# Performance work log

Measured on AMD Instinct MI355X. Metric: run time of the kernel, lower is better.

The kernel has to match this reference:

```python
import jax, jax.numpy as jnp
import numpy as np

N, DEG, D_FEAT, D_OUT = 50000, 32, 128, 256

def setup_inputs() -> dict:
    key = jax.random.key(0)
    k1, k2, k3 = jax.random.split(key, 3)
    features = jax.random.normal(k1, (N, D_FEAT), dtype=jnp.float32)
    edge_look_up = jax.random.randint(k2, (N, DEG), 0, N, dtype=jnp.int64)
    # glorot-uniform kernel, shape (2*D_FEAT, D_OUT)
    limit = np.sqrt(6.0 / (2 * D_FEAT + D_OUT)).astype(np.float32)
    kernel = jax.random.uniform(k3, (2 * D_FEAT, D_OUT), dtype=jnp.float32,
                                minval=-limit, maxval=limit)
    return {"features": features, "edge_look_up": edge_look_up, "kernel": kernel}

def reference(features, edge_look_up, kernel):
    # [1] neighborhood aggregation: gather neighbor features and mean-reduce
    neigh = features[edge_look_up]          # [N, DEG, D_FEAT] (irregular gather)
    agg = jnp.mean(neigh, axis=1)           # [N, D_FEAT]
    # [2] concat self features with aggregated neighbor vectors
    out = jnp.concatenate([features, agg], axis=-1)  # [N, 2*D_FEAT]
    # [4] dense matmul + [5] relu activation
    return jax.nn.relu(out @ kernel)        # [N, D_OUT]
```

## Files before the change

kernel.cpp:

```cpp
#include <hip/hip_runtime.h>

#define NN  50000
#define DEG 32
#define DF  128
#define DO  256
#define FEAT4 (NN * DF / 4)

typedef __bf16 bf16x8 __attribute__((ext_vector_type(8)));
typedef float  f32x4  __attribute__((ext_vector_type(4)));
typedef float  f32x2  __attribute__((ext_vector_type(2)));
typedef unsigned short u16x8 __attribute__((ext_vector_type(8)));

#if defined(__has_builtin)
#if __has_builtin(__builtin_amdgcn_cvt_pk_f32_fp8) && __has_builtin(__builtin_amdgcn_cvt_pk_fp8_f32)
#define HW_FP8 1
#endif
#endif
#ifndef HW_FP8
#define HW_FP8 0
#endif

__device__ __forceinline__ unsigned short f2bf(float f) {
    unsigned u = __float_as_uint(f);
    u += 0x7FFF + ((u >> 16) & 1);
    return (unsigned short)(u >> 16);
}

#if !HW_FP8
__device__ __forceinline__ unsigned enc1_fp8(float f) {
    unsigned u = __float_as_uint(f);
    unsigned s = (u >> 31) << 7;
    float a = fabsf(f);
    if (!(a > 0.f)) return s;
    if (a >= 448.f) return s | 0x7E;
    u = __float_as_uint(a);
    int e = (int)((u >> 23) & 255) - 127;
    if (e < -6) {
        unsigned m = (unsigned)(a * 512.f + 0.5f);
        if (m >= 8) return s | 0x08;
        return s | m;
    }
    unsigned mant = (u >> 20) & 7;
    unsigned rnd  = ((u >> 19) & 1) & (((u & 0x7FFFF) != 0) | ((u >> 20) & 1));
    unsigned enc  = ((unsigned)(e + 7) << 3) | mant;
    return s | (enc + rnd);
}
__device__ __forceinline__ float dec1_fp8(unsigned b) {
    unsigned s = (b >> 7) & 1, e = (b >> 3) & 15, m = b & 7;
    float v = (e == 0) ? (float)m * 0.001953125f
                       : __uint_as_float(((e - 7 + 127) << 23) | (m << 20));
    return s ? -v : v;
}
#endif

__device__ __forceinline__ unsigned enc4_fp8(float4 v) {
#if HW_FP8
    int pk = 0;
    pk = __builtin_amdgcn_cvt_pk_fp8_f32(v.x, v.y, pk, false);
    pk = __builtin_amdgcn_cvt_pk_fp8_f32(v.z, v.w, pk, true);
    return (unsigned)pk;
#else
    return enc1_fp8(v.x) | (enc1_fp8(v.y) << 8) | (enc1_fp8(v.z) << 16) | (enc1_fp8(v.w) << 24);
#endif
}

__global__ __launch_bounds__(256) void convert_kernel(
    const float* __restrict__ feat, const float* __restrict__ W,
    unsigned* __restrict__ feat8, unsigned short* __restrict__ featb,
    unsigned short* __restrict__ Wt)
{
    const int gid = blockIdx.x * 256 + threadIdx.x;
    if (gid < FEAT4) {
        const float4 v = ((const float4*)feat)[gid];
        feat8[gid] = enc4_fp8(v);
        ushort4 o;
        o.x = f2bf(v.x); o.y = f2bf(v.y); o.z = f2bf(v.z); o.w = f2bf(v.w);
        ((ushort4*)featb)[gid] = o;
    } else {
        const int t = gid - FEAT4;
        if (t < DO * DO) {
            const int n = t >> 8, k = t & 255;
            Wt[n * DO + k] = f2bf(W[k * DO + n]);
        }
    }
}

__global__ __launch_bounds__(256) void agg_kernel(
    const unsigned* __restrict__ feat8,
    const int*      __restrict__ edges,
    unsigned short* __restrict__ aggb)
{
    const int node = blockIdx.x * 16 + (threadIdx.x >> 4);
    const int l    = threadIdx.x & 15;
    const int* e   = edges + node * DEG;

    float a[8] = {0.f, 0.f, 0.f, 0.f, 0.f, 0.f, 0.f, 0.f};
    #pragma unroll
    for (int d = 0; d < DEG; ++d) {
        const int idx = e[d];
        const uint2 pk = *(const uint2*)(feat8 + (size_t)idx * (DF / 4) + l * 2);
#if HW_FP8
        const f32x2 v0 = __builtin_amdgcn_cvt_pk_f32_fp8((int)pk.x, false);
        const f32x2 v1 = __builtin_amdgcn_cvt_pk_f32_fp8((int)pk.x, true);
        const f32x2 v2 = __builtin_amdgcn_cvt_pk_f32_fp8((int)pk.y, false);
        const f32x2 v3 = __builtin_amdgcn_cvt_pk_f32_fp8((int)pk.y, true);
        a[0] += v0[0]; a[1] += v0[1]; a[2] += v1[0]; a[3] += v1[1];
        a[4] += v2[0]; a[5] += v2[1]; a[6] += v3[0]; a[7] += v3[1];
#else
        #pragma unroll
        for (int j = 0; j < 4; ++j) a[j]     += dec1_fp8((pk.x >> (8 * j)) & 255);
        #pragma unroll
        for (int j = 0; j < 4; ++j) a[4 + j] += dec1_fp8((pk.y >> (8 * j)) & 255);
#endif
    }

    const float s = 1.0f / (float)DEG;
    u16x8 o;
    #pragma unroll
    for (int j = 0; j < 8; ++j) o[j] = f2bf(a[j] * s);
    *(u16x8*)(aggb + (size_t)node * DF + l * 8) = o;
}

#define BM  64
#define BN  256
#define LDT 72

__global__ __launch_bounds__(512) void gemm_kernel(
    const unsigned short* __restrict__ featb,
    const unsigned short* __restrict__ aggb,
    const unsigned short* __restrict__ Wt,
    float*                __restrict__ out)
{
    __shared__ __align__(16) unsigned short Asw[BM * LDT];
    __shared__ __align__(16) unsigned short Bsw[BN * LDT];

    const int tid = threadIdx.x;
    const int m0  = blockIdx.x * BM;

    const int wave = tid >> 6, lane = tid & 63;
    const int quad = lane >> 4, lr = lane & 15;
    const int wm   = (wave & 1) * 32;
    const int wn   = (wave >> 1) * 64;

    f32x4 acc[2][4] = {};

    for (int kc = 0; kc < 4; ++kc) {
        const unsigned short* srcA = (kc < 2) ? (featb + kc * 64)
                                              : (aggb + (kc - 2) * 64);

        if (kc) __syncthreads();

        {
            const int r = tid >> 3;
            const int c = (tid & 7) * 8;
            int node = m0 + r;
            if (node >= NN) node = NN - 1;
            *(u16x8*)(Asw + r * LDT + c) =
                *(const u16x8*)(srcA + (size_t)node * DF + c);
        }

        #pragma unroll
        for (int it = 0; it < 4; ++it) {
            const int sidx = it * 512 + tid;
            const int r = sidx >> 3;
            const int c = (sidx & 7) * 8;
            *(u16x8*)(Bsw + r * LDT + c) =
                *(const u16x8*)(Wt + (size_t)r * DO + kc * 64 + c);
        }

        __syncthreads();

        #pragma unroll
        for (int kk = 0; kk < 64; kk += 32) {
            const int kb = kk + quad * 8;
            bf16x8 af[2], bfr[4];
            #pragma unroll
            for (int i = 0; i < 2; ++i)
                af[i] = *(const bf16x8*)(Asw + (wm + i * 16 + lr) * LDT + kb);
            #pragma unroll
            for (int i = 0; i < 4; ++i)
                bfr[i] = *(const bf16x8*)(Bsw + (wn + i * 16 + lr) * LDT + kb);
            #pragma unroll
            for (int mi = 0; mi < 2; ++mi)
                #pragma unroll
                for (int ni = 0; ni < 4; ++ni)
                    acc[mi][ni] = __builtin_amdgcn_mfma_f32_16x16x32_bf16(
                        af[mi], bfr[ni], acc[mi][ni], 0, 0, 0);
        }
    }

    #pragma unroll
    for (int mi = 0; mi < 2; ++mi) {
        #pragma unroll
        for (int r = 0; r < 4; ++r) {
            const int row = m0 + wm + mi * 16 + quad * 4 + r;
            if (row < NN) {
                #pragma unroll
                for (int ni = 0; ni < 4; ++ni) {
                    out[(size_t)row * DO + wn + ni * 16 + lr] =
                        fmaxf(acc[mi][ni][r], 0.f);
                }
            }
        }
    }
}

extern "C" void kernel_launch(void* const* d_in, const int* in_sizes, int n_in,
                              void* d_out, int out_size, void* d_ws, size_t ws_size,
                              hipStream_t stream)
{
    const float* feat  = (const float*)d_in[0];
    const int*   edges = (const int*)d_in[1];
    const float* W     = (const float*)d_in[2];
    float*       out   = (float*)d_out;

    unsigned short* aggb  = (unsigned short*)d_ws;
    unsigned*       feat8 = (unsigned*)(aggb + (size_t)NN * DF);
    unsigned short* featb = (unsigned short*)(feat8 + (size_t)NN * DF / 4);
    unsigned short* Wt    = featb + (size_t)NN * DF;

    convert_kernel<<<(FEAT4 + DO * DO + 255) / 256, 256, 0, stream>>>(
        feat, W, feat8, featb, Wt);
    agg_kernel<<<NN / 16, 256, 0, stream>>>(feat8, edges, aggb);

    gemm_kernel<<<(NN + BM - 1) / BM, 512, 0, stream>>>(featb, aggb, Wt, out);
}
```

Measured before the change: 124.6 us.

## Convert self features to bf16 inside GEMM and stage output through LDS

```diff
diff --git a/kernel.cpp b/kernel.cpp
--- a/kernel.cpp
+++ b/kernel.cpp
@@ -66,16 +66,12 @@
 
 __global__ __launch_bounds__(256) void convert_kernel(
     const float* __restrict__ feat, const float* __restrict__ W,
-    unsigned* __restrict__ feat8, unsigned short* __restrict__ featb,
-    unsigned short* __restrict__ Wt)
+    unsigned* __restrict__ feat8, unsigned short* __restrict__ Wt)
 {
     const int gid = blockIdx.x * 256 + threadIdx.x;
     if (gid < FEAT4) {
         const float4 v = ((const float4*)feat)[gid];
         feat8[gid] = enc4_fp8(v);
-        ushort4 o;
-        o.x = f2bf(v.x); o.y = f2bf(v.y); o.z = f2bf(v.z); o.w = f2bf(v.w);
-        ((ushort4*)featb)[gid] = o;
     } else {
         const int t = gid - FEAT4;
         if (t < DO * DO) {
@@ -124,9 +120,10 @@
 #define BM  64
 #define BN  256
 #define LDT 72
+#define LDP 68
 
 __global__ __launch_bounds__(512) void gemm_kernel(
-    const unsigned short* __restrict__ featb,
+    const float*          __restrict__ feat,
     const unsigned short* __restrict__ aggb,
     const unsigned short* __restrict__ Wt,
     float*                __restrict__ out)
@@ -145,9 +142,6 @@
     f32x4 acc[2][4] = {};
 
     for (int kc = 0; kc < 4; ++kc) {
-        const unsigned short* srcA = (kc < 2) ? (featb + kc * 64)
-                                              : (aggb + (kc - 2) * 64);
-
         if (kc) __syncthreads();
 
         {
@@ -155,8 +149,18 @@
             const int c = (tid & 7) * 8;
             int node = m0 + r;
             if (node >= NN) node = NN - 1;
-            *(u16x8*)(Asw + r * LDT + c) =
-                *(const u16x8*)(srcA + (size_t)node * DF + c);
+            if (kc < 2) {
+                const float* src = feat + (size_t)node * DF + kc * 64 + c;
+                const float4 v0 = *(const float4*)(src);
+                const float4 v1 = *(const float4*)(src + 4);
+                u16x8 o;
+                o[0] = f2bf(v0.x); o[1] = f2bf(v0.y); o[2] = f2bf(v0.z); o[3] = f2bf(v0.w);
+                o[4] = f2bf(v1.x); o[5] = f2bf(v1.y); o[6] = f2bf(v1.z); o[7] = f2bf(v1.w);
+                *(u16x8*)(Asw + r * LDT + c) = o;
+            } else {
+                *(u16x8*)(Asw + r * LDT + c) =
+                    *(const u16x8*)(aggb + (size_t)node * DF + (kc - 2) * 64 + c);
+            }
         }
 
         #pragma unroll
@@ -189,19 +193,31 @@
         }
     }
 
+    __syncthreads();
+    float* ws = (float*)Bsw + wave * (16 * LDP);
+
     #pragma unroll
     for (int mi = 0; mi < 2; ++mi) {
         #pragma unroll
-        for (int r = 0; r < 4; ++r) {
-            const int row = m0 + wm + mi * 16 + quad * 4 + r;
-            if (row < NN) {
-                #pragma unroll
-                for (int ni = 0; ni < 4; ++ni) {
-                    out[(size_t)row * DO + wn + ni * 16 + lr] =
-                        fmaxf(acc[mi][ni][r], 0.f);
-                }
-            }
-        }
+        for (int ni = 0; ni < 4; ++ni)
+            #pragma unroll
+            for (int r = 0; r < 4; ++r)
+                ws[(quad * 4 + r) * LDP + ni * 16 + lr] =
+                    fmaxf(acc[mi][ni][r], 0.f);
+
+        __syncthreads();
+
+        #pragma unroll
+        for (int p = 0; p < 4; ++p) {
+            const int row = p * 4 + (lane >> 4);
+            const int cg  = (lane & 15) * 4;
+            const float4 v = *(const float4*)(ws + row * LDP + cg);
+            const int grow = m0 + wm + mi * 16 + row;
+            if (grow < NN)
+                *(float4*)(out + (size_t)grow * DO + wn + cg) = v;
+        }
+
+        __syncthreads();
     }
 }
 
@@ -216,12 +232,11 @@
 
     unsigned short* aggb  = (unsigned short*)d_ws;
     unsigned*       feat8 = (unsigned*)(aggb + (size_t)NN * DF);
-    unsigned short* featb = (unsigned short*)(feat8 + (size_t)NN * DF / 4);
-    unsigned short* Wt    = featb + (size_t)NN * DF;
+    unsigned short* Wt    = (unsigned short*)(feat8 + (size_t)NN * DF / 4);
 
     convert_kernel<<<(FEAT4 + DO * DO + 255) / 256, 256, 0, stream>>>(
-        feat, W, feat8, featb, Wt);
+        feat, W, feat8, Wt);
     agg_kernel<<<NN / 16, 256, 0, stream>>>(feat8, edges, aggb);
 
-    gemm_kernel<<<(NN + BM - 1) / BM, 512, 0, stream>>>(featb, aggb, Wt, out);
-}
+    gemm_kernel<<<(NN + BM - 1) / BM, 512, 0, stream>>>(feat, aggb, Wt, out);
+}
```

New measurement: 124.1 us. No clear change (-0.4%).
